# Performance work log

Hardware: AMD Instinct MI355X
Metric: run time of the kernel (lower is better)

## Reference

```python
import jax, jax.numpy as jnp
import numpy as np

EEG_CH = 64      # eeg_channel_new
WIN = 128        # window_length
KEN = 10         # cnn_ken_num
CONV_H = 64      # cnn_conv_hight (stride/kernel height)


def setup_inputs() -> dict:
    key = jax.random.key(0)
    ks = jax.random.split(key, 11)
    n = jax.random.normal
    return {
        "x": n(ks[0], (1, 1, 66, 128), dtype=jnp.float32),
        # SE fcn: Linear(64,64) -> Tanh -> Linear(64,64) -> Sigmoid -> Softmax
        "se_w1": n(ks[1], (64, 64), dtype=jnp.float32) * 0.1,
        "se_b1": n(ks[2], (64,), dtype=jnp.float32) * 0.1,
        "se_w2": n(ks[3], (64, 64), dtype=jnp.float32) * 0.1,
        "se_b2": n(ks[4], (64,), dtype=jnp.float32) * 0.1,
        # Conv2d(1, 10, (64, 9), stride=(64, 1))
        "conv_w": n(ks[5], (10, 1, 64, 9), dtype=jnp.float32) * 0.05,
        "conv_b": n(ks[6], (10,), dtype=jnp.float32) * 0.05,
        # fcn: Linear(20,10) -> Sigmoid -> Linear(10,2) -> Softmax
        "fcn_w1": n(ks[7], (10, 20), dtype=jnp.float32) * 0.1,
        "fcn_b1": n(ks[8], (10,), dtype=jnp.float32) * 0.1,
        "fcn_w2": n(ks[9], (2, 10), dtype=jnp.float32) * 0.1,
        "fcn_b2": n(ks[10], (2,), dtype=jnp.float32) * 0.1,
    }


def _dot(a, b):
    # Faithful to torch: tensordot over dim 0 -> [64,1]; diag of non-square -> [1];
    # then broadcast-divide by per-column norms -> [64].
    temp = jnp.diagonal(jnp.tensordot(a, b, axes=[[0], [0]]))  # [1]
    norm_a = jnp.linalg.norm(a, axis=0)                        # [64]
    norm_b = jnp.linalg.norm(b, axis=0)                        # [1]
    return temp / (norm_a * norm_b)                            # [64]


def reference(x, se_w1, se_b1, se_w2, se_b2, conv_w, conv_b,
              fcn_w1, fcn_b1, fcn_w2, fcn_b2):
    eeg = x[:, :, 1:1 + EEG_CH, :]      # [1,1,64,128]
    wav_a = x[:, :, 0:1, :]             # [1,1,1,128]
    wav_b = x[:, :, -1:, :]             # [1,1,1,128]

    e2 = eeg.reshape(EEG_CH, WIN)       # [64,128]
    r_a = _dot(e2.T, wav_a.reshape(1, WIN).T)   # [64]
    r_b = _dot(e2.T, wav_b.reshape(1, WIN).T)   # [64]
    eeg_r = jnp.concatenate([r_a, r_b]).reshape(2, -1)  # [2,64]

    # SE channel attention
    h = jnp.tanh(eeg_r @ se_w1.T + se_b1)
    se_w = jax.nn.softmax(jax.nn.sigmoid(h @ se_w2.T + se_b2), axis=1)  # [2,64]
    sd = eeg.reshape(1, EEG_CH, WIN).transpose(1, 0, 2)  # [64,1,128]
    sd = jnp.concatenate([sd, sd], axis=0)               # [128,1,128]
    # (transpose(0,2) * w.view(1,-1)).transpose(0,2) == scale along doubled-channel dim
    eeg_se = (sd * se_w.reshape(-1)[:, None, None]).transpose(1, 0, 2)  # [1,128,128]

    y = eeg_se.reshape(1, 1, 2 * EEG_CH, WIN)            # [1,1,128,128]
    y = jax.lax.conv_general_dilated(
        y, conv_w, window_strides=(CONV_H, 1), padding='VALID',
        dimension_numbers=('NCHW', 'OIHW', 'NCHW'))       # [1,10,2,120]
    y = jax.nn.relu(y + conv_b[None, :, None, None])
    # AdaptiveAvgPool2d((2,1)): H already 2, mean over W
    y = jnp.mean(y, axis=3, keepdims=True)                # [1,10,2,1]
    y = y.reshape(1, -1)                                  # [1,20]

    h2 = jax.nn.sigmoid(y @ fcn_w1.T + fcn_b1)
    return jax.nn.softmax(h2 @ fcn_w2.T + fcn_b2, axis=1)  # [1,2]
```

## Files before the change

### kernel.cpp

```cpp
#include <hip/hip_runtime.h>
#include <math.h>

#define EEG_CH 64
#define WIN    128
#define KW     9
#define OUTW   120
#define NOUT   10
#define ROWP   132

__device__ float        g_msum[2 * NOUT];
__device__ unsigned int g_ctr = 0;

__device__ __forceinline__ float readlane_f(float v, int l) {
    return __int_as_float(__builtin_amdgcn_readlane(__float_as_int(v), l));
}

__launch_bounds__(1024)
__global__ void cnn_fused(const float* __restrict__ xg,
                          const float* __restrict__ w1g, const float* __restrict__ b1g,
                          const float* __restrict__ w2g, const float* __restrict__ b2g,
                          const float* __restrict__ cwg, const float* __restrict__ cbg,
                          const float* __restrict__ f1w, const float* __restrict__ f1b,
                          const float* __restrict__ f2w, const float* __restrict__ f2b,
                          float* __restrict__ out)
{
    __shared__ float w1l[64 * 64];
    __shared__ float w2l[64 * 64];
    __shared__ float xl[64 * ROWP];
    __shared__ float rnorm[66];
    __shared__ float nums[2];
    __shared__ float sef[128];
    __shared__ float part[4][OUTW];
    __shared__ float msh[2];
    __shared__ int   sflag;
    __shared__ float msums[2 * NOUT];

    const int tid  = threadIdx.x;
    const int wv   = tid >> 6;
    const int lane = tid & 63;
    const int o    = blockIdx.x;

    for (int t = tid; t < 2048; t += 1024) {
        const int row = t >> 5, c4 = t & 31;
        const float4 v = *(const float4*)(xg + (row + 1) * WIN + c4 * 4);
        *(float4*)(xl + row * ROWP + c4 * 4) = v;
    }
    for (int t = tid; t < 2048; t += 1024) {
        const int j  = t & 63;
        const int i4 = (t >> 6) & 15;
        const float* __restrict__ src = (t < 1024) ? w1g : w2g;
        float* __restrict__ dst = (t < 1024) ? w1l : w2l;
        const float4 v = *(const float4*)(src + j * 64 + i4 * 4);
        dst[(i4 * 4 + 0) * 64 + j] = v.x;
        dst[(i4 * 4 + 1) * 64 + j] = v.y;
        dst[(i4 * 4 + 2) * 64 + j] = v.z;
        dst[(i4 * 4 + 3) * 64 + j] = v.w;
    }
    const int h = wv >> 1, ihalf = wv & 1;
    const int chbase = ihalf * 32;
    float wl[KW];
    if (wv < 4 && lane < 32) {
        const float* __restrict__ cwo = cwg + o * (EEG_CH * KW) + (chbase + lane) * KW;
        #pragma unroll
        for (int k = 0; k < KW; ++k) wl[k] = cwo[k];
    }
    for (int row = wv; row < 66; row += 16) {
        const float v0 = xg[row * WIN + lane];
        const float v1 = xg[row * WIN + 64 + lane];
        float s = v0 * v0 + v1 * v1;
        for (int off = 32; off > 0; off >>= 1) s += __shfl_xor(s, off, 64);
        if (lane == 0) rnorm[row] = sqrtf(s);
    }
    if (wv < 2) {
        const int wrow = (wv == 0) ? 0 : 65;
        float p = xg[WIN + lane]      * xg[wrow * WIN + lane]
                + xg[WIN + 64 + lane] * xg[wrow * WIN + 64 + lane];
        for (int off = 32; off > 0; off >>= 1) p += __shfl_xor(p, off, 64);
        if (lane == 0) nums[wv] = p;
    }
    __syncthreads();

    if (wv < 2) {
        const int r = wv, j = lane;
        const float er = nums[r] / (rnorm[j + 1] * (r == 0 ? rnorm[0] : rnorm[65]));
        float acc = b1g[j];
        #pragma unroll
        for (int i = 0; i < 64; ++i)
            acc += readlane_f(er, i) * w1l[i * 64 + j];
        const float hv = tanhf(acc);
        float acc2 = b2g[j];
        #pragma unroll
        for (int i = 0; i < 64; ++i)
            acc2 += readlane_f(hv, i) * w2l[i * 64 + j];
        const float sg = 1.f / (1.f + expf(-acc2));
        float mx = sg;
        for (int off = 32; off > 0; off >>= 1) mx = fmaxf(mx, __shfl_xor(mx, off, 64));
        const float e = expf(sg - mx);
        float ss = e;
        for (int off = 32; off > 0; off >>= 1) ss += __shfl_xor(ss, off, 64);
        sef[r * 64 + j] = e / ss;
    }
    __syncthreads();

    const int wbase = (lane < 60) ? 2 * lane : 116;
    if (wv < 4) {
        float sl = 0.f;
        if (lane < 32) sl = sef[h * 64 + chbase + lane];

        float q0 = 0.f, q1 = 0.f;
        #pragma unroll 4
        for (int ii = 0; ii < 32; ++ii) {
            const int i = chbase + ii;
            const float2* xp = (const float2*)(xl + i * ROWP + wbase);
            const float2 x0 = xp[0], x1 = xp[1], x2 = xp[2], x3 = xp[3], x4 = xp[4];
            const float xw[10] = { x0.x, x0.y, x1.x, x1.y, x2.x, x2.y,
                                   x3.x, x3.y, x4.x, x4.y };
            float wk[KW];
            #pragma unroll
            for (int k = 0; k < KW; ++k) wk[k] = readlane_f(wl[k], ii);
            const float s = readlane_f(sl, ii);
            float p0 = 0.f, p1 = 0.f;
            #pragma unroll
            for (int k = 0; k < KW; ++k) {
                p0 += xw[k]     * wk[k];
                p1 += xw[k + 1] * wk[k];
            }
            q0 += s * p0;
            q1 += s * p1;
        }
        if (lane < 60) {
            *(float2*)(&part[wv][wbase]) = make_float2(q0, q1);
        }
    }
    __syncthreads();

    if (wv < 2) {
        const float bo = cbg[o];
        float r = 0.f;
        if (lane < 60) {
            const float v0 = part[wv * 2][wbase]     + part[wv * 2 + 1][wbase]     + bo;
            const float v1 = part[wv * 2][wbase + 1] + part[wv * 2 + 1][wbase + 1] + bo;
            r = fmaxf(v0, 0.f) + fmaxf(v1, 0.f);
        }
        for (int off = 32; off > 0; off >>= 1) r += __shfl_xor(r, off, 64);
        if (lane == 0) msh[wv] = r * (1.0f / OUTW);
    }
    __syncthreads();

    if (tid == 0) {
        __hip_atomic_store(&g_msum[o * 2 + 0], msh[0], __ATOMIC_RELAXED, __HIP_MEMORY_SCOPE_AGENT);
        __hip_atomic_store(&g_msum[o * 2 + 1], msh[1], __ATOMIC_RELAXED, __HIP_MEMORY_SCOPE_AGENT);
        const unsigned old = __hip_atomic_fetch_add(&g_ctr, 1u, __ATOMIC_ACQ_REL, __HIP_MEMORY_SCOPE_AGENT);
        sflag = (old % 10u == 9u) ? 1 : 0;
    }
    __syncthreads();

    if (sflag) {
        if (tid < 2 * NOUT)
            msums[tid] = __hip_atomic_load(&g_msum[tid], __ATOMIC_ACQUIRE, __HIP_MEMORY_SCOPE_AGENT);
        __syncthreads();
        if (tid < 64) {
            float h2v = 0.f;
            if (lane < 10) {
                float a = f1b[lane];
                #pragma unroll
                for (int p = 0; p < 20; ++p) a += msums[p] * f1w[lane * 20 + p];
                h2v = 1.f / (1.f + expf(-a));
            }
            float t0 = (lane < 10) ? h2v * f2w[lane]      : 0.f;
            float t1 = (lane < 10) ? h2v * f2w[10 + lane] : 0.f;
            for (int off = 32; off > 0; off >>= 1) {
                t0 += __shfl_xor(t0, off, 64);
                t1 += __shfl_xor(t1, off, 64);
            }
            if (lane == 0) {
                const float l0 = f2b[0] + t0, l1 = f2b[1] + t1;
                const float m  = fmaxf(l0, l1);
                const float e0 = expf(l0 - m), e1 = expf(l1 - m);
                out[0] = e0 / (e0 + e1);
                out[1] = e1 / (e0 + e1);
            }
        }
    }
}

extern "C" void kernel_launch(void* const* d_in, const int* in_sizes, int n_in,
                              void* d_out, int out_size, void* d_ws, size_t ws_size,
                              hipStream_t stream) {
    (void)in_sizes; (void)n_in; (void)ws_size; (void)out_size; (void)d_ws;
    const float* xg  = (const float*)d_in[0];
    const float* w1  = (const float*)d_in[1];
    const float* b1  = (const float*)d_in[2];
    const float* w2  = (const float*)d_in[3];
    const float* b2  = (const float*)d_in[4];
    const float* cw  = (const float*)d_in[5];
    const float* cb  = (const float*)d_in[6];
    const float* f1w = (const float*)d_in[7];
    const float* f1b = (const float*)d_in[8];
    const float* f2w = (const float*)d_in[9];
    const float* f2b = (const float*)d_in[10];
    float* out = (float*)d_out;

    cnn_fused<<<dim3(NOUT), dim3(1024), 0, stream>>>(xg, w1, b1, w2, b2,
                                                     cw, cb, f1w, f1b, f2w, f2b, out);
}
```

Measured before the change: 84.54 us.

## Spread conv across all 16 waves and do per-wave completion signaling

The convolution work moves from 4 waves of 32 channels each to all 16 waves of 8 channels each, with 16 partial rows reduced by two waves. The final cross-block handshake becomes per-wave: each reducing wave stores its mean and bumps the global counter itself, so two block-wide syncs and shared flags go away. The 20th arrival runs the final FC layers. This shortens the serial per-wave inner loop but adds more partial-sum traffic and twice as many global atomics.

```diff
diff --git a/kernel.cpp b/kernel.cpp
--- a/kernel.cpp
+++ b/kernel.cpp
@@ -30,16 +30,22 @@
     __shared__ float rnorm[66];
     __shared__ float nums[2];
     __shared__ float sef[128];
-    __shared__ float part[4][OUTW];
-    __shared__ float msh[2];
-    __shared__ int   sflag;
-    __shared__ float msums[2 * NOUT];
+    __shared__ float part[16][OUTW];
 
     const int tid  = threadIdx.x;
     const int wv   = tid >> 6;
     const int lane = tid & 63;
     const int o    = blockIdx.x;
 
+    const int h      = wv >> 3;
+    const int chbase = (wv & 7) * 8;
+
+    float wl[KW];
+    if (lane < 8) {
+        const float* __restrict__ cwo = cwg + o * (EEG_CH * KW) + (chbase + lane) * KW;
+        #pragma unroll
+        for (int k = 0; k < KW; ++k) wl[k] = cwo[k];
+    }
     for (int t = tid; t < 2048; t += 1024) {
         const int row = t >> 5, c4 = t & 31;
         const float4 v = *(const float4*)(xg + (row + 1) * WIN + c4 * 4);
@@ -56,14 +62,6 @@
         dst[(i4 * 4 + 2) * 64 + j] = v.z;
         dst[(i4 * 4 + 3) * 64 + j] = v.w;
     }
-    const int h = wv >> 1, ihalf = wv & 1;
-    const int chbase = ihalf * 32;
-    float wl[KW];
-    if (wv < 4 && lane < 32) {
-        const float* __restrict__ cwo = cwg + o * (EEG_CH * KW) + (chbase + lane) * KW;
-        #pragma unroll
-        for (int k = 0; k < KW; ++k) wl[k] = cwo[k];
-    }
     for (int row = wv; row < 66; row += 16) {
         const float v0 = xg[row * WIN + lane];
         const float v1 = xg[row * WIN + 64 + lane];
@@ -103,13 +101,13 @@
     __syncthreads();
 
     const int wbase = (lane < 60) ? 2 * lane : 116;
-    if (wv < 4) {
+    {
         float sl = 0.f;
-        if (lane < 32) sl = sef[h * 64 + chbase + lane];
+        if (lane < 8) sl = sef[h * 64 + chbase + lane];
 
         float q0 = 0.f, q1 = 0.f;
-        #pragma unroll 4
-        for (int ii = 0; ii < 32; ++ii) {
+        #pragma unroll
+        for (int ii = 0; ii < 8; ++ii) {
             const int i = chbase + ii;
             const float2* xp = (const float2*)(xl + i * ROWP + wbase);
             const float2 x0 = xp[0], x1 = xp[1], x2 = xp[2], x3 = xp[3], x4 = xp[4];
@@ -138,33 +136,37 @@
         const float bo = cbg[o];
         float r = 0.f;
         if (lane < 60) {
-            const float v0 = part[wv * 2][wbase]     + part[wv * 2 + 1][wbase]     + bo;
-            const float v1 = part[wv * 2][wbase + 1] + part[wv * 2 + 1][wbase + 1] + bo;
+            float v0 = part[wv * 8][wbase],     v1 = part[wv * 8][wbase + 1];
+            #pragma unroll
+            for (int q = 1; q < 8; ++q) {
+                v0 += part[wv * 8 + q][wbase];
+                v1 += part[wv * 8 + q][wbase + 1];
+            }
+            v0 += bo; v1 += bo;
             r = fmaxf(v0, 0.f) + fmaxf(v1, 0.f);
         }
         for (int off = 32; off > 0; off >>= 1) r += __shfl_xor(r, off, 64);
-        if (lane == 0) msh[wv] = r * (1.0f / OUTW);
-    }
-    __syncthreads();
-
-    if (tid == 0) {
-        __hip_atomic_store(&g_msum[o * 2 + 0], msh[0], __ATOMIC_RELAXED, __HIP_MEMORY_SCOPE_AGENT);
-        __hip_atomic_store(&g_msum[o * 2 + 1], msh[1], __ATOMIC_RELAXED, __HIP_MEMORY_SCOPE_AGENT);
-        const unsigned old = __hip_atomic_fetch_add(&g_ctr, 1u, __ATOMIC_ACQ_REL, __HIP_MEMORY_SCOPE_AGENT);
-        sflag = (old % 10u == 9u) ? 1 : 0;
-    }
-    __syncthreads();
-
-    if (sflag) {
-        if (tid < 2 * NOUT)
-            msums[tid] = __hip_atomic_load(&g_msum[tid], __ATOMIC_ACQUIRE, __HIP_MEMORY_SCOPE_AGENT);
-        __syncthreads();
-        if (tid < 64) {
+
+        unsigned old = 0u;
+        if (lane == 0) {
+            __hip_atomic_store(&g_msum[o * 2 + wv], r * (1.0f / OUTW),
+                               __ATOMIC_RELAXED, __HIP_MEMORY_SCOPE_AGENT);
+            old = __hip_atomic_fetch_add(&g_ctr, 1u, __ATOMIC_ACQ_REL,
+                                         __HIP_MEMORY_SCOPE_AGENT) + 1u;
+        }
+        const unsigned myord = (unsigned)__builtin_amdgcn_readlane((int)old, 0);
+
+        if (myord % 20u == 0u && myord != 0u) {
+            float msumv = 0.f;
+            if (lane < 2 * NOUT)
+                msumv = __hip_atomic_load(&g_msum[lane], __ATOMIC_ACQUIRE,
+                                          __HIP_MEMORY_SCOPE_AGENT);
             float h2v = 0.f;
             if (lane < 10) {
                 float a = f1b[lane];
                 #pragma unroll
-                for (int p = 0; p < 20; ++p) a += msums[p] * f1w[lane * 20 + p];
+                for (int p = 0; p < 20; ++p)
+                    a += readlane_f(msumv, p) * f1w[lane * 20 + p];
                 h2v = 1.f / (1.f + expf(-a));
             }
             float t0 = (lane < 10) ? h2v * f2w[lane]      : 0.f;
```

Measured after the change: 85.53 us. About the same (+1.2%).
